# Optimization experiments

Measured on AMD Instinct MI355X. Metric: run time of the kernel, lower is better.

## Reference

```python
import jax, jax.numpy as jnp
import numpy as np

DIM = 768
HEADS = 12
HEAD_DIM = DIM // HEADS
SCALE = HEAD_DIM ** -0.5
BATCH = 4      # B videos
FRAMES = 64    # f frames
NTOK = 128     # W_TP tokens per window


def setup_inputs() -> dict:
    key = jax.random.key(0)
    ks = jax.random.split(key, 6)
    x = jax.random.normal(ks[0], (BATCH * FRAMES, NTOK, DIM), jnp.float32)
    # binary mask per frame (zeros are later masked_fill'd to -10000)
    mask = (jax.random.uniform(ks[1], (FRAMES, NTOK, NTOK)) > 0.2).astype(jnp.float32)
    edge_bias = jax.random.normal(ks[2], (NTOK, NTOK), jnp.float32)
    qkv_w = jax.random.normal(ks[3], (3 * DIM, DIM), jnp.float32) * (DIM ** -0.5)
    qkv_b = jnp.zeros((3 * DIM,), jnp.float32)
    proj_w = jax.random.normal(ks[4], (DIM, DIM), jnp.float32) * (DIM ** -0.5)
    proj_b = jnp.zeros((DIM,), jnp.float32)
    return {"x": x, "mask": mask, "edge_bias": edge_bias,
            "qkv_w": qkv_w, "qkv_b": qkv_b,
            "proj_w": proj_w, "proj_b": proj_b,
            "B": BATCH, "f": FRAMES}


def reference(x, mask, edge_bias, qkv_w, qkv_b, proj_w, proj_b, B, f):
    B_f, N, D = x.shape
    H, Dh = HEADS, D // HEADS
    # qkv projection -> [3, B_f, H, N, Dh]
    qkv = (x @ qkv_w.T + qkv_b).reshape(B_f, N, 3, H, Dh)
    qkv = jnp.transpose(qkv, (2, 0, 3, 1, 4))
    q = qkv[0] * jnp.float32(SCALE)
    k = qkv[1]
    v = qkv[2]
    # raw scores [B_f, H, N, N]
    attn = jnp.einsum('bhnd,bhmd->bhnm', q, k)
    # mask multiply ([1,f,1,N,N]) and edge-bias multiply ([1,1,1,N,N])
    attn = attn.reshape(B, f, H, N, N)
    attn = attn * mask[None, :, None] * edge_bias[None, None, None]
    attn = attn.reshape(B_f, H, N, N)
    # masked_fill(attn == 0, -10000) then softmax of NEGATED scores
    attn = jnp.where(attn == 0.0, jnp.float32(-10000.0), attn)
    attn = jax.nn.softmax(-attn, axis=-1)
    out = jnp.einsum('bhnm,bhmd->bhnd', attn, v)  # [B_f,H,N,Dh]
    out = jnp.transpose(out, (0, 2, 1, 3)).reshape(B_f, N, D)
    return out @ proj_w.T + proj_b
```

## Files before the change

kernel.cpp:

```cpp
#include <hip/hip_runtime.h>

typedef unsigned short u16;
typedef unsigned int   u32;
typedef unsigned long long u64;

typedef __attribute__((ext_vector_type(8))) short bf16x8;
typedef __attribute__((ext_vector_type(4))) float f32x4;
typedef __attribute__((ext_vector_type(4))) unsigned int u32x4;

__device__ __forceinline__ u16 rne_bf16(float f) {
  u32 u = __builtin_bit_cast(u32, f);
  u = (u + 0x7fffu + ((u >> 16) & 1u)) >> 16;
  return (u16)u;
}
__device__ __forceinline__ u32 pack_bf16x2(float lo, float hi) {
  return (u32)rne_bf16(lo) | ((u32)rne_bf16(hi) << 16);
}
__device__ __forceinline__ u32 cvt_pk_bf16(float lo, float hi) {
  u32 r;
  asm volatile("v_cvt_pk_bf16_f32 %0, %1, %2" : "=v"(r) : "v"(lo), "v"(hi));
  return r;
}

__global__ __launch_bounds__(256)
void prep_small(const float* __restrict__ mask,
                const float* __restrict__ proj_w, const float* __restrict__ qkv_b,
                const float* __restrict__ proj_b,
                u64* __restrict__ bm0, u64* __restrict__ bm1,
                float* __restrict__ invc, float* __restrict__ cbias) {
  const int b = blockIdx.x;
  const int lane = threadIdx.x & 63;
  if (b < 2048) {
    int row = b * 4 + (threadIdx.x >> 6);
    float v0 = mask[(long)row * 128 + lane];
    float v1 = mask[(long)row * 128 + 64 + lane];
    u64 b0 = __ballot(v0 == 0.0f);
    u64 b1 = __ballot(v1 == 0.0f);
    if (lane == 0) {
      bm0[row] = b0; bm1[row] = b1;
      int c = __builtin_popcountll(b0) + __builtin_popcountll(b1);
      invc[row] = c ? (1.0f / (float)c) : 0.0f;
    }
  } else {
    int i = (b - 2048) * 4 + (threadIdx.x >> 6);
    float s = 0.f;
    for (int j = lane; j < 768; j += 64) s += proj_w[(long)i * 768 + j] * qkv_b[1536 + j];
    #pragma unroll
    for (int off = 32; off; off >>= 1) s += __shfl_down(s, off);
    if (lane == 0) cbias[i] = s + proj_b[i];
  }
}

__global__ __launch_bounds__(256)
void transpose_wv(const float* __restrict__ qkv_w, u16* __restrict__ WvT) {
  __shared__ float tile[64][65];
  int tj = blockIdx.x % 12, td = blockIdx.x / 12;
  int t = threadIdx.x;
  const float* src = qkv_w + (long)1536 * 768 + (long)(tj * 64) * 768 + td * 64;
  #pragma unroll
  for (int i = 0; i < 4; ++i) {
    int j = (t >> 4) + 16 * i;
    int d = (t & 15) * 4;
    float4 v = *(const float4*)&src[(long)j * 768 + d];
    tile[j][d] = v.x; tile[j][d + 1] = v.y; tile[j][d + 2] = v.z; tile[j][d + 3] = v.w;
  }
  __syncthreads();
  u16* dst = WvT + (long)(td * 64) * 768 + tj * 64;
  #pragma unroll
  for (int i = 0; i < 4; ++i) {
    int d = (t >> 4) + 16 * i;
    int j = (t & 15) * 4;
    uint2 p;
    p.x = pack_bf16x2(tile[j][d],     tile[j + 1][d]);
    p.y = pack_bf16x2(tile[j + 2][d], tile[j + 3][d]);
    *(uint2*)&dst[(long)d * 768 + j] = p;
  }
}

template<bool A_FP32, bool B_FP32, bool BF16_OUT>
__global__ __launch_bounds__(256, 4)
void gemm_bt(const void* __restrict__ Av, const void* __restrict__ Bv,
             void* __restrict__ Cv, const float* __restrict__ bias,
             int M, int N, int K, int nblk) {
  __shared__ u16 lA[2][128 * 32];
  __shared__ u16 lB[2][128 * 32];

  const int nwg = gridDim.x;
  const int bid = blockIdx.x;
  const int qq = nwg >> 3, rr8 = nwg & 7;
  const int xcd = bid & 7, loc = bid >> 3;
  const int swz = (xcd < rr8) ? (xcd * (qq + 1) + loc)
                              : (rr8 * (qq + 1) + (xcd - rr8) * qq + loc);
  const int mb = swz / nblk, nb = swz % nblk;
  const long arow0 = (long)mb * 128;
  const long brow0 = (long)nb * 128;

  const int tid = threadIdx.x;
  const int lane = tid & 63, wid = tid >> 6;
  const int wr = wid >> 1, wc = wid & 1;

  const int nk = K >> 5;

  f32x4 acc[4][4];
  const f32x4 vzero = {0.f, 0.f, 0.f, 0.f};
  #pragma unroll
  for (int i = 0; i < 4; ++i)
    #pragma unroll
    for (int j = 0; j < 4; ++j) acc[i][j] = vzero;

  auto stage = [&](int buf, int kt) {
    if constexpr (B_FP32) {
      const float* Bf = (const float*)Bv;
      #pragma unroll
      for (int i = 0; i < 4; ++i) {
        int row = 32 * i + (tid >> 3);
        int kk = 4 * (tid & 7);
        float4 v = *(const float4*)&Bf[(brow0 + row) * (long)K + kt * 32 + kk];
        uint2 p; p.x = pack_bf16x2(v.x, v.y); p.y = pack_bf16x2(v.z, v.w);
        int byte = row * 64 + ((8 * (tid & 7)) ^ (((row >> 1) & 3) << 4));
        *(uint2*)((char*)&lB[buf][0] + byte) = p;
      }
    } else {
      const u16* Bb = (const u16*)Bv;
      #pragma unroll
      for (int i = 0; i < 2; ++i) {
        int tt = tid + 256 * i;
        int gsrc = (tt & 3) ^ ((tt >> 3) & 3);
        const u16* g = &Bb[(brow0 + (tt >> 2)) * (long)K + kt * 32 + 8 * gsrc];
        __builtin_amdgcn_global_load_lds(
            static_cast<const u32*>(static_cast<const void*>(g)),
            static_cast<u32*>(static_cast<void*>(&lB[buf][512 * wid + 2048 * i])),
            16, 0, 0);
      }
    }
    if constexpr (A_FP32) {
      const float* Af = (const float*)Av;
      #pragma unroll
      for (int i = 0; i < 4; ++i) {
        int row = 32 * i + (tid >> 3);
        int kk = 4 * (tid & 7);
        float4 v = *(const float4*)&Af[(arow0 + row) * (long)K + kt * 32 + kk];
        uint2 p; p.x = pack_bf16x2(v.x, v.y); p.y = pack_bf16x2(v.z, v.w);
        int byte = row * 64 + ((8 * (tid & 7)) ^ (((row >> 1) & 3) << 4));
        *(uint2*)((char*)&lA[buf][0] + byte) = p;
      }
    } else {
      const u16* Ab = (const u16*)Av;
      #pragma unroll
      for (int i = 0; i < 2; ++i) {
        int tt = tid + 256 * i;
        int gsrc = (tt & 3) ^ ((tt >> 3) & 3);
        const u16* g = &Ab[(arow0 + (tt >> 2)) * (long)K + kt * 32 + 8 * gsrc];
        __builtin_amdgcn_global_load_lds(
            static_cast<const u32*>(static_cast<const void*>(g)),
            static_cast<u32*>(static_cast<void*>(&lA[buf][512 * wid + 2048 * i])),
            16, 0, 0);
      }
    }
  };

  stage(0, 0);
  __syncthreads();

  int cur = 0;
  for (int kt = 0; kt < nk; ++kt) {
    if (kt + 1 < nk) stage(cur ^ 1, kt + 1);
    bf16x8 afr[4], bfr[4];
    #pragma unroll
    for (int i = 0; i < 4; ++i) {
      int ra = 64 * wr + 16 * i + (lane & 15);
      afr[i] = *(const bf16x8*)((const char*)&lA[cur][0] +
                ra * 64 + ((16 * (lane >> 4)) ^ (((ra >> 1) & 3) << 4)));
      int rb = 64 * wc + 16 * i + (lane & 15);
      bfr[i] = *(const bf16x8*)((const char*)&lB[cur][0] +
                rb * 64 + ((16 * (lane >> 4)) ^ (((rb >> 1) & 3) << 4)));
    }
    #pragma unroll
    for (int b = 0; b < 4; ++b)
      #pragma unroll
      for (int a = 0; a < 4; ++a)
        acc[b][a] = __builtin_amdgcn_mfma_f32_16x16x32_bf16(bfr[b], afr[a], acc[b][a], 0, 0, 0);
    __syncthreads();
    cur ^= 1;
  }

  #pragma unroll
  for (int b = 0; b < 4; ++b) {
    long n0 = brow0 + 64 * wc + 16 * b + 4 * (lane >> 4);
    #pragma unroll
    for (int a = 0; a < 4; ++a) {
      long m = arow0 + 64 * wr + 16 * a + (lane & 15);
      if constexpr (BF16_OUT) {
        uint2 p;
        p.x = pack_bf16x2(acc[b][a][0], acc[b][a][1]);
        p.y = pack_bf16x2(acc[b][a][2], acc[b][a][3]);
        *(uint2*)&((u16*)Cv)[m * N + n0] = p;
      } else {
        const float4 bb = *(const float4*)&bias[n0];
        float4 o;
        o.x = acc[b][a][0] + bb.x; o.y = acc[b][a][1] + bb.y;
        o.z = acc[b][a][2] + bb.z; o.w = acc[b][a][3] + bb.w;
        *(float4*)&((float*)Cv)[m * N + n0] = o;
      }
    }
  }
}

__global__ __launch_bounds__(512, 6)
void msa_fused(const u16* __restrict__ Wc, const float* __restrict__ x,
               const u64* __restrict__ bm0, const u64* __restrict__ bm1,
               const float* __restrict__ invc, const float* __restrict__ cbias,
               float* __restrict__ out) {
  __shared__ alignas(16) char smem[51200];
  u16*   lA  = (u16*)smem;
  char*  lBf = smem + 16384;
  u64*   lbm = (u64*)(smem + 49152);
  u16*   lYT = (u16*)smem;

  const int bid = blockIdx.x;
  const int swz = (bid & 7) * 192 + (bid >> 3);
  const int bfi  = swz / 6;
  const int iblk = swz - 6 * bfi;
  const int fr   = bfi & 63;
  const long arow0 = (long)iblk * 128;
  const long brow0 = (long)bfi * 128;

  const int tid = threadIdx.x;
  const int lane = tid & 63, wid = tid >> 6;
  const int wr = wid >> 2, wc = wid & 3;

  if (tid < 128) {
    lbm[2 * tid]     = bm0[fr * 128 + tid];
    lbm[2 * tid + 1] = bm1[fr * 128 + tid];
  }

  f32x4 acc[2][4];
  const f32x4 vzero = {0.f, 0.f, 0.f, 0.f};
  #pragma unroll
  for (int i = 0; i < 2; ++i)
    #pragma unroll
    for (int j = 0; j < 4; ++j) acc[i][j] = vzero;

  auto stage = [&](int buf, int kt) {
    {
      int gsrc = (tid & 3) ^ ((tid >> 3) & 3);
      const u16* g = &Wc[(arow0 + (tid >> 2)) * 768L + kt * 32 + 8 * gsrc];
      __builtin_amdgcn_global_load_lds(
          static_cast<const u32*>(static_cast<const void*>(g)),
          static_cast<u32*>(static_cast<void*>(lA + buf * 4096 + 512 * wid)),
          16, 0, 0);
    }
    #pragma unroll
    for (int i = 0; i < 2; ++i) {
      int G = i * 512 + tid;
      int r = G >> 3;
      int gl = (G & 7) ^ (r & 7);
      const float* g = &x[(brow0 + r) * 768L + kt * 32 + 4 * gl];
      __builtin_amdgcn_global_load_lds(
          static_cast<const u32*>(static_cast<const void*>(g)),
          static_cast<u32*>(static_cast<void*>(lBf + buf * 16384 + i * 8192 + wid * 1024 + lane * 16)),
          16, 0, 0);
    }
  };

  stage(0, 0);
  __syncthreads();

  const int q = lane >> 4;
  int cur = 0;
  for (int kt = 0; kt < 24; ++kt) {
    if (kt + 1 < 24) stage(cur ^ 1, kt + 1);
    bf16x8 afr[4], bfr[2];
    #pragma unroll
    for (int i = 0; i < 4; ++i) {
      int ra = 64 * wr + 16 * i + (lane & 15);
      afr[i] = *(const bf16x8*)((const char*)(lA + cur * 4096) +
                ra * 64 + ((16 * q) ^ (((ra >> 1) & 3) << 4)));
    }
    #pragma unroll
    for (int i = 0; i < 2; ++i) {
      int t = 32 * wc + 16 * i + (lane & 15);
      const char* base = lBf + cur * 16384 + t * 128;
      f32x4 lo = *(const f32x4*)(base + 16 * ((2 * q) ^ (t & 7)));
      f32x4 hi = *(const f32x4*)(base + 16 * ((2 * q + 1) ^ (t & 7)));
      u32x4 wv;
      wv.x = cvt_pk_bf16(lo[0], lo[1]);
      wv.y = cvt_pk_bf16(lo[2], lo[3]);
      wv.z = cvt_pk_bf16(hi[0], hi[1]);
      wv.w = cvt_pk_bf16(hi[2], hi[3]);
      bfr[i] = __builtin_bit_cast(bf16x8, wv);
    }
    #pragma unroll
    for (int b = 0; b < 2; ++b)
      #pragma unroll
      for (int a = 0; a < 4; ++a)
        acc[b][a] = __builtin_amdgcn_mfma_f32_16x16x32_bf16(bfr[b], afr[a], acc[b][a], 0, 0, 0);
    __syncthreads();
    cur ^= 1;
  }

  #pragma unroll
  for (int b = 0; b < 2; ++b) {
    int mq = 32 * wc + 16 * b + 4 * q;
    #pragma unroll
    for (int a = 0; a < 4; ++a) {
      int i = 64 * wr + 16 * a + (lane & 15);
      uint2 p;
      p.x = pack_bf16x2(acc[b][a][0], acc[b][a][1]);
      p.y = pack_bf16x2(acc[b][a][2], acc[b][a][3]);
      int sw = (i & 15) ^ ((i >> 4) & 3);
      int byte = i * 256 + (((mq >> 3) ^ sw) << 4) + (mq & 7) * 2;
      *(uint2*)((char*)lYT + byte) = p;
    }
  }
  __syncthreads();

  f32x4 acc2[4][2];
  #pragma unroll
  for (int i = 0; i < 4; ++i)
    #pragma unroll
    for (int j = 0; j < 2; ++j) acc2[i][j] = vzero;

  const unsigned char* lbmB = (const unsigned char*)lbm;
  #pragma unroll
  for (int kk = 0; kk < 4; ++kk) {
    int klog = 64 * kk + 16 * q;
    bf16x8 yfr[4], mfr[2];
    #pragma unroll
    for (int ii = 0; ii < 4; ++ii) {
      int i = 64 * wr + 16 * ii + (lane & 15);
      int sw = ((i & 15) ^ ((i >> 4) & 3)) << 4;
      yfr[ii] = *(const bf16x8*)((char*)lYT + i * 256 + (klog ^ sw));
    }
    #pragma unroll
    for (int tt = 0; tt < 2; ++tt) {
      int t = 32 * wc + 16 * tt + (lane & 15);
      u32 b8 = lbmB[t * 16 + 4 * kk + q];
      u32x4 wv;
      wv.x = ((b8 & 1)  ? 0x3f80u : 0u) | ((b8 & 2)   ? 0x3f800000u : 0u);
      wv.y = ((b8 & 4)  ? 0x3f80u : 0u) | ((b8 & 8)   ? 0x3f800000u : 0u);
      wv.z = ((b8 & 16) ? 0x3f80u : 0u) | ((b8 & 32)  ? 0x3f800000u : 0u);
      wv.w = ((b8 & 64) ? 0x3f80u : 0u) | ((b8 & 128) ? 0x3f800000u : 0u);
      mfr[tt] = __builtin_bit_cast(bf16x8, wv);
    }
    #pragma unroll
    for (int ii = 0; ii < 4; ++ii)
      #pragma unroll
      for (int tt = 0; tt < 2; ++tt)
        acc2[ii][tt] = __builtin_amdgcn_mfma_f32_16x16x32_bf16(yfr[ii], mfr[tt], acc2[ii][tt], 0, 0, 0);
  }

  const float* icp = invc + fr * 128;
  float icv[2];
  #pragma unroll
  for (int tt = 0; tt < 2; ++tt) icv[tt] = icp[32 * wc + 16 * tt + (lane & 15)];
  #pragma unroll
  for (int ii = 0; ii < 4; ++ii) {
    int i0 = iblk * 128 + 64 * wr + 16 * ii + 4 * q;
    float4 cb4 = *(const float4*)&cbias[i0];
    #pragma unroll
    for (int tt = 0; tt < 2; ++tt) {
      long tok = brow0 + 32 * wc + 16 * tt + (lane & 15);
      float4 o;
      o.x = acc2[ii][tt][0] * icv[tt] + cb4.x;
      o.y = acc2[ii][tt][1] * icv[tt] + cb4.y;
      o.z = acc2[ii][tt][2] * icv[tt] + cb4.z;
      o.w = acc2[ii][tt][3] * icv[tt] + cb4.w;
      *(float4*)&out[tok * 768 + i0] = o;
    }
  }
}

extern "C" void kernel_launch(void* const* d_in, const int* in_sizes, int n_in,
                              void* d_out, int out_size, void* d_ws, size_t ws_size,
                              hipStream_t stream) {
  (void)in_sizes; (void)n_in; (void)out_size; (void)ws_size;
  const float* x      = (const float*)d_in[0];
  const float* mask   = (const float*)d_in[1];
  const float* qkv_w  = (const float*)d_in[3];
  const float* qkv_b  = (const float*)d_in[4];
  const float* proj_w = (const float*)d_in[5];
  const float* proj_b = (const float*)d_in[6];

  char* w = (char*)d_ws;
  u16*   WvT  = (u16*)(w);
  u16*   Wc   = (u16*)(w + 0x120000);
  float* cb   = (float*)(w + 0x240000);
  u64*   bm0  = (u64*)(w + 0x241000);
  u64*   bm1  = (u64*)(w + 0x251000);
  float* invc = (float*)(w + 0x261000);

  prep_small<<<dim3(2240), dim3(256), 0, stream>>>(mask, proj_w, qkv_b, proj_b,
                                                   bm0, bm1, invc, cb);
  transpose_wv<<<dim3(144), dim3(256), 0, stream>>>(qkv_w, WvT);
  gemm_bt<true, false, true><<<dim3(36), dim3(256), 0, stream>>>(
      (const void*)proj_w, (const void*)WvT, (void*)Wc, nullptr, 768, 768, 768, 6);
  msa_fused<<<dim3(1536), dim3(512), 0, stream>>>(Wc, x, bm0, bm1, invc, cb, (float*)d_out);
}
```

Baseline: 110.8 us.

## Triple-buffer the fused QKV GEMM loads with one barrier per k-step

Changes the GEMM main loop in the fused attention kernel from double to triple buffering of the LDS tiles. Two stages are prefetched ahead, and explicit vmcnt waits plus a single barrier per iteration replace the trailing __syncthreads. The goal is to hide global-to-LDS latency and remove one barrier per iteration. In exchange, LDS per block grows by roughly half and the launch-bounds occupancy hint drops, which lowers the number of resident blocks.

New measurement: 112.4 us. No clear change (+1.4%).

```diff
diff --git a/kernel.cpp b/kernel.cpp
--- a/kernel.cpp
+++ b/kernel.cpp
@@ -206,16 +206,14 @@
   }
 }
 
-__global__ __launch_bounds__(512, 6)
+__global__ __launch_bounds__(512, 4)
 void msa_fused(const u16* __restrict__ Wc, const float* __restrict__ x,
                const u64* __restrict__ bm0, const u64* __restrict__ bm1,
                const float* __restrict__ invc, const float* __restrict__ cbias,
                float* __restrict__ out) {
-  __shared__ alignas(16) char smem[51200];
-  u16*   lA  = (u16*)smem;
-  char*  lBf = smem + 16384;
-  u64*   lbm = (u64*)(smem + 49152);
-  u16*   lYT = (u16*)smem;
+  __shared__ alignas(16) char smem[75776];
+  u64* lbm = (u64*)(smem + 73728);
+  u16* lYT = (u16*)smem;
 
   const int bid = blockIdx.x;
   const int swz = (bid & 7) * 192 + (bid >> 3);
@@ -242,12 +240,13 @@
     for (int j = 0; j < 4; ++j) acc[i][j] = vzero;
 
   auto stage = [&](int buf, int kt) {
+    char* base = smem + buf * 24576;
     {
       int gsrc = (tid & 3) ^ ((tid >> 3) & 3);
       const u16* g = &Wc[(arow0 + (tid >> 2)) * 768L + kt * 32 + 8 * gsrc];
       __builtin_amdgcn_global_load_lds(
           static_cast<const u32*>(static_cast<const void*>(g)),
-          static_cast<u32*>(static_cast<void*>(lA + buf * 4096 + 512 * wid)),
+          static_cast<u32*>(static_cast<void*>(base + 1024 * wid)),
           16, 0, 0);
     }
     #pragma unroll
@@ -258,31 +257,36 @@
       const float* g = &x[(brow0 + r) * 768L + kt * 32 + 4 * gl];
       __builtin_amdgcn_global_load_lds(
           static_cast<const u32*>(static_cast<const void*>(g)),
-          static_cast<u32*>(static_cast<void*>(lBf + buf * 16384 + i * 8192 + wid * 1024 + lane * 16)),
+          static_cast<u32*>(static_cast<void*>(base + 8192 + i * 8192 + 1024 * wid + 16 * lane)),
           16, 0, 0);
     }
   };
 
   stage(0, 0);
-  __syncthreads();
+  stage(1, 1);
 
   const int q = lane >> 4;
-  int cur = 0;
+  int cur = 0, nxt = 2;
   for (int kt = 0; kt < 24; ++kt) {
-    if (kt + 1 < 24) stage(cur ^ 1, kt + 1);
+    if (kt < 23) { asm volatile("s_waitcnt vmcnt(3)" ::: "memory"); }
+    else         { asm volatile("s_waitcnt vmcnt(0)" ::: "memory"); }
+    __builtin_amdgcn_s_barrier();
+    __builtin_amdgcn_sched_barrier(0);
+    if (kt + 2 < 24) stage(nxt, kt + 2);
+
+    const char* base = smem + cur * 24576;
     bf16x8 afr[4], bfr[2];
     #pragma unroll
     for (int i = 0; i < 4; ++i) {
       int ra = 64 * wr + 16 * i + (lane & 15);
-      afr[i] = *(const bf16x8*)((const char*)(lA + cur * 4096) +
-                ra * 64 + ((16 * q) ^ (((ra >> 1) & 3) << 4)));
+      afr[i] = *(const bf16x8*)(base + ra * 64 + ((16 * q) ^ (((ra >> 1) & 3) << 4)));
     }
     #pragma unroll
     for (int i = 0; i < 2; ++i) {
       int t = 32 * wc + 16 * i + (lane & 15);
-      const char* base = lBf + cur * 16384 + t * 128;
-      f32x4 lo = *(const f32x4*)(base + 16 * ((2 * q) ^ (t & 7)));
-      f32x4 hi = *(const f32x4*)(base + 16 * ((2 * q + 1) ^ (t & 7)));
+      const char* b2 = base + 8192 + t * 128;
+      f32x4 lo = *(const f32x4*)(b2 + 16 * ((2 * q) ^ (t & 7)));
+      f32x4 hi = *(const f32x4*)(b2 + 16 * ((2 * q + 1) ^ (t & 7)));
       u32x4 wv;
       wv.x = cvt_pk_bf16(lo[0], lo[1]);
       wv.y = cvt_pk_bf16(lo[2], lo[3]);
@@ -295,8 +299,9 @@
       #pragma unroll
       for (int a = 0; a < 4; ++a)
         acc[b][a] = __builtin_amdgcn_mfma_f32_16x16x32_bf16(bfr[b], afr[a], acc[b][a], 0, 0, 0);
-    __syncthreads();
-    cur ^= 1;
+
+    cur = (cur == 2) ? 0 : cur + 1;
+    nxt = (nxt == 2) ? 0 : nxt + 1;
   }
 
   #pragma unroll
```

## Load GEMM operands directly from global memory into registers, dropping LDS staging

Applied to the files above, without the earlier changes.

The first GEMM stage of the fused kernel no longer uses double-buffered global_load_lds staging of the weight and x tiles into shared memory. Each wave now reads its MFMA fragments straight from global memory into registers every k-step, with no barriers. LDS use shrinks from 51200 to 34816 bytes, which can allow more resident blocks and removes the per-iteration syncs. In exchange, operands shared between waves are read redundantly from global/L2, there is no software prefetch, and the loads are less coalesced, so load latency may be exposed.

New measurement: 324.8 us. 2.93x slower.

```diff
diff --git a/kernel.cpp b/kernel.cpp
--- a/kernel.cpp
+++ b/kernel.cpp
@@ -211,11 +211,9 @@
                const u64* __restrict__ bm0, const u64* __restrict__ bm1,
                const float* __restrict__ invc, const float* __restrict__ cbias,
                float* __restrict__ out) {
-  __shared__ alignas(16) char smem[51200];
-  u16*   lA  = (u16*)smem;
-  char*  lBf = smem + 16384;
-  u64*   lbm = (u64*)(smem + 49152);
-  u16*   lYT = (u16*)smem;
+  __shared__ alignas(16) char smem[34816];
+  u16* lYT = (u16*)smem;
+  u64* lbm = (u64*)(smem + 32768);
 
   const int bid = blockIdx.x;
   const int swz = (bid & 7) * 192 + (bid >> 3);
@@ -228,6 +226,7 @@
   const int tid = threadIdx.x;
   const int lane = tid & 63, wid = tid >> 6;
   const int wr = wid >> 2, wc = wid & 3;
+  const int q = lane >> 4, l15 = lane & 15;
 
   if (tid < 128) {
     lbm[2 * tid]     = bm0[fr * 128 + tid];
@@ -241,62 +240,33 @@
     #pragma unroll
     for (int j = 0; j < 4; ++j) acc[i][j] = vzero;
 
-  auto stage = [&](int buf, int kt) {
-    {
-      int gsrc = (tid & 3) ^ ((tid >> 3) & 3);
-      const u16* g = &Wc[(arow0 + (tid >> 2)) * 768L + kt * 32 + 8 * gsrc];
-      __builtin_amdgcn_global_load_lds(
-          static_cast<const u32*>(static_cast<const void*>(g)),
-          static_cast<u32*>(static_cast<void*>(lA + buf * 4096 + 512 * wid)),
-          16, 0, 0);
-    }
-    #pragma unroll
-    for (int i = 0; i < 2; ++i) {
-      int G = i * 512 + tid;
-      int r = G >> 3;
-      int gl = (G & 7) ^ (r & 7);
-      const float* g = &x[(brow0 + r) * 768L + kt * 32 + 4 * gl];
-      __builtin_amdgcn_global_load_lds(
-          static_cast<const u32*>(static_cast<const void*>(g)),
-          static_cast<u32*>(static_cast<void*>(lBf + buf * 16384 + i * 8192 + wid * 1024 + lane * 16)),
-          16, 0, 0);
-    }
-  };
-
-  stage(0, 0);
-  __syncthreads();
-
-  const int q = lane >> 4;
-  int cur = 0;
+  const u16*   aBase = Wc + (arow0 + 64 * wr + l15) * 768L + 8 * q;
+  const float* bBase = x  + (brow0 + 32 * wc + l15) * 768L + 8 * q;
+
   for (int kt = 0; kt < 24; ++kt) {
-    if (kt + 1 < 24) stage(cur ^ 1, kt + 1);
-    bf16x8 afr[4], bfr[2];
-    #pragma unroll
-    for (int i = 0; i < 4; ++i) {
-      int ra = 64 * wr + 16 * i + (lane & 15);
-      afr[i] = *(const bf16x8*)((const char*)(lA + cur * 4096) +
-                ra * 64 + ((16 * q) ^ (((ra >> 1) & 3) << 4)));
-    }
-    #pragma unroll
-    for (int i = 0; i < 2; ++i) {
-      int t = 32 * wc + 16 * i + (lane & 15);
-      const char* base = lBf + cur * 16384 + t * 128;
-      f32x4 lo = *(const f32x4*)(base + 16 * ((2 * q) ^ (t & 7)));
-      f32x4 hi = *(const f32x4*)(base + 16 * ((2 * q + 1) ^ (t & 7)));
+    bf16x8 afr[4];
+    f32x4  blo[2], bhi[2];
+    #pragma unroll
+    for (int i = 0; i < 4; ++i)
+      afr[i] = *(const bf16x8*)(aBase + 16L * i * 768 + kt * 32);
+    #pragma unroll
+    for (int j = 0; j < 2; ++j) {
+      const float* p = bBase + 16L * j * 768 + kt * 32;
+      blo[j] = *(const f32x4*)(p);
+      bhi[j] = *(const f32x4*)(p + 4);
+    }
+    #pragma unroll
+    for (int j = 0; j < 2; ++j) {
       u32x4 wv;
-      wv.x = cvt_pk_bf16(lo[0], lo[1]);
-      wv.y = cvt_pk_bf16(lo[2], lo[3]);
-      wv.z = cvt_pk_bf16(hi[0], hi[1]);
-      wv.w = cvt_pk_bf16(hi[2], hi[3]);
-      bfr[i] = __builtin_bit_cast(bf16x8, wv);
-    }
-    #pragma unroll
-    for (int b = 0; b < 2; ++b)
+      wv.x = cvt_pk_bf16(blo[j][0], blo[j][1]);
+      wv.y = cvt_pk_bf16(blo[j][2], blo[j][3]);
+      wv.z = cvt_pk_bf16(bhi[j][0], bhi[j][1]);
+      wv.w = cvt_pk_bf16(bhi[j][2], bhi[j][3]);
+      bf16x8 bfr = __builtin_bit_cast(bf16x8, wv);
       #pragma unroll
       for (int a = 0; a < 4; ++a)
-        acc[b][a] = __builtin_amdgcn_mfma_f32_16x16x32_bf16(bfr[b], afr[a], acc[b][a], 0, 0, 0);
-    __syncthreads();
-    cur ^= 1;
+        acc[j][a] = __builtin_amdgcn_mfma_f32_16x16x32_bf16(bfr, afr[a], acc[j][a], 0, 0, 0);
+    }
   }
 
   #pragma unroll
@@ -304,7 +274,7 @@
     int mq = 32 * wc + 16 * b + 4 * q;
     #pragma unroll
     for (int a = 0; a < 4; ++a) {
-      int i = 64 * wr + 16 * a + (lane & 15);
+      int i = 64 * wr + 16 * a + l15;
       uint2 p;
       p.x = pack_bf16x2(acc[b][a][0], acc[b][a][1]);
       p.y = pack_bf16x2(acc[b][a][2], acc[b][a][3]);
@@ -328,13 +298,13 @@
     bf16x8 yfr[4], mfr[2];
     #pragma unroll
     for (int ii = 0; ii < 4; ++ii) {
-      int i = 64 * wr + 16 * ii + (lane & 15);
+      int i = 64 * wr + 16 * ii + l15;
       int sw = ((i & 15) ^ ((i >> 4) & 3)) << 4;
       yfr[ii] = *(const bf16x8*)((char*)lYT + i * 256 + (klog ^ sw));
     }
     #pragma unroll
     for (int tt = 0; tt < 2; ++tt) {
-      int t = 32 * wc + 16 * tt + (lane & 15);
+      int t = 32 * wc + 16 * tt + l15;
       u32 b8 = lbmB[t * 16 + 4 * kk + q];
       u32x4 wv;
       wv.x = ((b8 & 1)  ? 0x3f80u : 0u) | ((b8 & 2)   ? 0x3f800000u : 0u);
@@ -353,14 +323,14 @@
   const float* icp = invc + fr * 128;
   float icv[2];
   #pragma unroll
-  for (int tt = 0; tt < 2; ++tt) icv[tt] = icp[32 * wc + 16 * tt + (lane & 15)];
+  for (int tt = 0; tt < 2; ++tt) icv[tt] = icp[32 * wc + 16 * tt + l15];
   #pragma unroll
   for (int ii = 0; ii < 4; ++ii) {
     int i0 = iblk * 128 + 64 * wr + 16 * ii + 4 * q;
     float4 cb4 = *(const float4*)&cbias[i0];
     #pragma unroll
     for (int tt = 0; tt < 2; ++tt) {
-      long tok = brow0 + 32 * wc + 16 * tt + (lane & 15);
+      long tok = brow0 + 32 * wc + 16 * tt + l15;
       float4 o;
       o.x = acc2[ii][tt][0] * icv[tt] + cb4.x;
       o.y = acc2[ii][tt][1] * icv[tt] + cb4.y;
```
